# Kernel optimization log

Measured on AMD Instinct MI355X. Metric: run time of the kernel, lower is better.

## Reference

```python
import jax, jax.numpy as jnp
import numpy as np

N = 100000   # nodes
F_IN = 128   # node features
H = 32       # hidden size (hard-coded in module)


def setup_inputs() -> dict:
    key = jax.random.key(0)
    ks = jax.random.split(key, 20)
    inp = {
        'x': jax.random.normal(ks[0], (N, F_IN), dtype=jnp.float32),
        'edge_index': jax.random.randint(ks[1], (2, 3200000), 0, N, dtype=jnp.int64),
        'edge_weight': jax.random.uniform(ks[2], (3200000,), dtype=jnp.float32),
        'prev_hidden_state': jax.random.normal(ks[3], (N, H), dtype=jnp.float32),
    }
    s = 1.0 / np.sqrt(F_IN)
    s2 = 1.0 / np.sqrt(2 * H)
    sh = 1.0 / np.sqrt(H)
    # GCNConv weights (in->H) + bias, for gates z, r, h
    for i, g in enumerate(['z', 'r', 'h']):
        inp[f'Wc_{g}'] = jax.random.uniform(ks[4 + i], (F_IN, H), minval=-s, maxval=s, dtype=jnp.float32)
        inp[f'bc_{g}'] = jnp.zeros((H,), dtype=jnp.float32)
        # torch Linear(2H -> H): weight [H, 2H], bias [H]
        inp[f'Wl_{g}'] = jax.random.uniform(ks[8 + i], (H, 2 * H), minval=-s2, maxval=s2, dtype=jnp.float32)
        inp[f'bl_{g}'] = jax.random.uniform(ks[12 + i], (H,), minval=-s2, maxval=s2, dtype=jnp.float32)
    inp['W_head'] = jax.random.uniform(ks[16], (1, H), minval=-sh, maxval=sh, dtype=jnp.float32)
    inp['b_head'] = jax.random.uniform(ks[17], (1,), minval=-sh, maxval=sh, dtype=jnp.float32)
    return inp


def _gcn_norm(edge_index, edge_weight):
    # add self-loops with weight 1, symmetric GCN normalization
    loop = jnp.arange(N, dtype=edge_index.dtype)
    row = jnp.concatenate([edge_index[0], loop])
    col = jnp.concatenate([edge_index[1], loop])
    w = jnp.concatenate([edge_weight, jnp.ones((N,), dtype=edge_weight.dtype)])
    deg = jax.ops.segment_sum(w, col, num_segments=N)
    dinv = jnp.where(deg > 0, jax.lax.rsqrt(jnp.where(deg > 0, deg, 1.0)), 0.0)
    norm = dinv[row] * w * dinv[col]
    return row, col, norm


def _gcn_conv(x, W, b, row, col, norm):
    xw = x @ W                                   # [N, H]
    agg = jax.ops.segment_sum(norm[:, None] * xw[row], col, num_segments=N)
    return agg + b


def reference(x, edge_index, edge_weight, prev_hidden_state,
              Wc_z, bc_z, Wl_z, bl_z,
              Wc_r, bc_r, Wl_r, bl_r,
              Wc_h, bc_h, Wl_h, bl_h,
              W_head, b_head):
    row, col, norm = _gcn_norm(edge_index, edge_weight)
    Hprev = prev_hidden_state

    cz = _gcn_conv(x, Wc_z, bc_z, row, col, norm)
    Z = jax.nn.sigmoid(jnp.concatenate([cz, Hprev], axis=1) @ Wl_z.T + bl_z)

    cr = _gcn_conv(x, Wc_r, bc_r, row, col, norm)
    R = jax.nn.sigmoid(jnp.concatenate([cr, Hprev], axis=1) @ Wl_r.T + bl_r)

    ch = _gcn_conv(x, Wc_h, bc_h, row, col, norm)
    Ht = jnp.tanh(jnp.concatenate([ch, Hprev * R], axis=1) @ Wl_h.T + bl_h)

    Hnew = Z * Hprev + (1.0 - Z) * Ht
    y = jax.nn.relu(Hnew) @ W_head.T + b_head    # [N, 1]
    return (y, Hnew)
```

## Files before the change

### kernel.cpp

```cpp
#include <hip/hip_runtime.h>

#define NN 100000
#define FIN 128
#define HD 32
#define EE 3200000
#define NBUK 391
#define EPB 6144
#define NBLK ((EE + EPB - 1) / EPB)

typedef unsigned int uint;
typedef unsigned short ushort;
typedef float vfloat4 __attribute__((ext_vector_type(4)));

__device__ __forceinline__ ushort f2bf(float f) {
    uint b = __float_as_uint(f);
    return (ushort)((b + 0x7FFFu + ((b >> 16) & 1u)) >> 16);
}
__device__ __forceinline__ float bf2f(ushort u) {
    return __uint_as_float(((uint)u) << 16);
}

__device__ __forceinline__ int load_idx32(const int* __restrict__ ei, long long pos, int is64) {
    return is64 ? __builtin_nontemporal_load(ei + pos * 2)
                : __builtin_nontemporal_load(ei + pos);
}

__global__ __launch_bounds__(256) void passA_hist(const int* __restrict__ ei,
                                                  int* __restrict__ blockhist,
                                                  int* __restrict__ flag) {
    __shared__ int hist[NBUK];
    __shared__ int sis64;
    int tid = threadIdx.x, blk = blockIdx.x;
    for (int b = tid; b < NBUK; b += 256) hist[b] = 0;
    if (tid < 64) {
        uint v = 0;
#pragma unroll
        for (int r = 0; r < 4; r++) v |= ((const uint*)ei)[2 * (tid + 64 * r) + 1];
        unsigned long long nz = __ballot(v != 0u);
        if (tid == 0) sis64 = (nz == 0ULL) ? 1 : 0;
    }
    __syncthreads();
    int is64 = sis64;
    if (blk == 0 && tid == 0) *flag = is64;
    int e0 = blk * EPB, e1 = e0 + EPB; if (e1 > EE) e1 = EE;
    for (int e = e0 + tid; e < e1; e += 256) {
        int col = load_idx32(ei, (long long)EE + e, is64);
        atomicAdd(&hist[col >> 8], 1);
    }
    __syncthreads();
    for (int b = tid; b < NBUK; b += 256) blockhist[blk * NBUK + b] = hist[b];
}

__global__ void scan_bucket(const int* __restrict__ blockhist, int* __restrict__ off_local,
                            int* __restrict__ total) {
    int b = blockIdx.x;
    int l = threadIdx.x;
    int run = 0;
    for (int c = 0; c < NBLK; c += 64) {
        int blk = c + l;
        int v = (blk < NBLK) ? blockhist[blk * NBUK + b] : 0;
        int incl = v;
#pragma unroll
        for (int d = 1; d < 64; d <<= 1) {
            int t = __shfl_up(incl, d, 64);
            if (l >= d) incl += t;
        }
        if (blk < NBLK) off_local[blk * NBUK + b] = run + (incl - v);
        run += __shfl(incl, 63, 64);
    }
    if (l == 0) total[b] = run;
}

__global__ void scan_total(const int* __restrict__ total, int* __restrict__ bstart) {
    __shared__ int sd[512];
    int t = threadIdx.x;
    int v = (t < NBUK) ? total[t] : 0;
    sd[t] = v;
    __syncthreads();
    for (int off = 1; off < 512; off <<= 1) {
        int x = (t >= off) ? sd[t - off] : 0;
        __syncthreads();
        sd[t] += x;
        __syncthreads();
    }
    if (t < NBUK) bstart[t] = sd[t] - v;
    if (t == NBUK - 1) bstart[NBUK] = sd[t];
}

__global__ __launch_bounds__(512) void sortC_kernel(const int* __restrict__ ei,
                                                    const float* __restrict__ wt,
                                                    const int* __restrict__ bstart,
                                                    const int* __restrict__ off_local,
                                                    const int* __restrict__ blockhist,
                                                    uint2* __restrict__ erec2,
                                                    const int* __restrict__ flag) {
    __shared__ uint2 lrec[EPB];
    __shared__ int lcombo[NBUK];
    __shared__ int lcur[NBUK];
    int tid = threadIdx.x, blk = blockIdx.x;
    if (tid < 64) {
        int run = 0;
        for (int c = 0; c < NBUK; c += 64) {
            int b = c + tid;
            int v = (b < NBUK) ? blockhist[blk * NBUK + b] : 0;
            int incl = v;
#pragma unroll
            for (int d = 1; d < 64; d <<= 1) {
                int t2 = __shfl_up(incl, d, 64);
                if (tid >= d) incl += t2;
            }
            if (b < NBUK) {
                int ls = run + incl - v;
                lcur[b] = ls;
                lcombo[b] = bstart[b] + off_local[blk * NBUK + b] - ls;
            }
            run += __shfl(incl, 63, 64);
        }
    }
    __syncthreads();
    int is64 = *flag;
    int e0 = blk * EPB, e1 = e0 + EPB; if (e1 > EE) e1 = EE;
    for (int e = e0 + tid; e < e1; e += 512) {
        int row = load_idx32(ei, e, is64);
        int col = load_idx32(ei, (long long)EE + e, is64);
        uint nb = __float_as_uint(__builtin_nontemporal_load(wt + e));
        uint enc = ((nb + 0x8000u) >> 16) & 0x7FFFu;
        int pos = atomicAdd(&lcur[col >> 8], 1);
        uint2 r; r.x = (uint)row | (enc << 17); r.y = (uint)col;
        lrec[pos] = r;
    }
    __syncthreads();
    int m = e1 - e0;
    for (int slot = tid; slot < m; slot += 512) {
        uint2 r = lrec[slot];
        int gpos = lcombo[r.y >> 8] + slot;
        erec2[gpos] = r;
    }
}

__global__ __launch_bounds__(512) void passB_fine(const uint2* __restrict__ erec2,
                                                  const int* __restrict__ bstart,
                                                  uint* __restrict__ erecF,
                                                  int* __restrict__ estart, int* __restrict__ cnt,
                                                  float* __restrict__ dinv) {
    __shared__ int hist[256];
    __shared__ float wsum[256];
    __shared__ int off[256];
    __shared__ int cur[256];
    __shared__ int sd[256];
    int t = threadIdx.x, b = blockIdx.x;
    if (t < 256) { hist[t] = 0; wsum[t] = 0.f; }
    __syncthreads();
    int e0 = bstart[b], e1 = bstart[b + 1];
    for (int e = e0 + t; e < e1; e += 512) {
        uint2 r = erec2[e];
        int cl = (int)(r.y & 255u);
        atomicAdd(&hist[cl], 1);
        atomicAdd(&wsum[cl], __uint_as_float((r.x >> 17) << 16));
    }
    __syncthreads();
    int v = 0;
    if (t < 256) { v = hist[t]; sd[t] = v; }
    __syncthreads();
    for (int o = 1; o < 256; o <<= 1) {
        int x = (t >= o && t < 256) ? sd[t - o] : 0;
        __syncthreads();
        if (t < 256) sd[t] += x;
        __syncthreads();
    }
    if (t < 256) {
        off[t] = sd[t] - v;
        cur[t] = 0;
        int node = b * 256 + t;
        if (node < NN) {
            estart[node] = e0 + off[t];
            cnt[node] = v;
            dinv[node] = rsqrtf(1.0f + wsum[t]);
        }
    }
    __syncthreads();
    for (int e = e0 + t; e < e1; e += 512) {
        uint2 r = erec2[e];
        int cl = (int)(r.y & 255u);
        int p = atomicAdd(&cur[cl], 1);
        erecF[e0 + off[cl] + p] = r.x;
    }
}

__global__ __launch_bounds__(256) void gemm_xw_kernel(
        const float* __restrict__ x,
        const float* __restrict__ Wz, const float* __restrict__ Wr, const float* __restrict__ Wh,
        const float* __restrict__ dinv,
        ushort* __restrict__ xw16) {
    __shared__ float Bs[128 * 96];
    __shared__ float AsT[8 * 128];
    int tid = threadIdx.x;
    int tx = tid & 31, ty = tid >> 5;
    int rowBase = blockIdx.x * 128;

    for (int e = tid; e < 4096; e += 256) { int k = e >> 5, c = e & 31; Bs[k * 96 + c]      = Wz[e]; }
    for (int e = tid; e < 4096; e += 256) { int k = e >> 5, c = e & 31; Bs[k * 96 + 32 + c] = Wr[e]; }
    for (int e = tid; e < 4096; e += 256) { int k = e >> 5, c = e & 31; Bs[k * 96 + 64 + c] = Wh[e]; }

    float acc0[16], acc1[16], acc2[16];
#pragma unroll
    for (int r = 0; r < 16; r++) { acc0[r] = 0.f; acc1[r] = 0.f; acc2[r] = 0.f; }

    int lr = tid >> 1;
    int lc = (tid & 1) * 4;
    for (int k0 = 0; k0 < 128; k0 += 8) {
        __syncthreads();
        int gr = rowBase + lr;
        vfloat4 a4 = (vfloat4)(0.f);
        if (gr < NN) a4 = __builtin_nontemporal_load((const vfloat4*)(x + (long long)gr * FIN + k0 + lc));
        AsT[(lc + 0) * 128 + lr] = a4.x;
        AsT[(lc + 1) * 128 + lr] = a4.y;
        AsT[(lc + 2) * 128 + lr] = a4.z;
        AsT[(lc + 3) * 128 + lr] = a4.w;
        __syncthreads();
#pragma unroll
        for (int kk = 0; kk < 8; kk++) {
            float b0 = Bs[(k0 + kk) * 96 + tx];
            float b1 = Bs[(k0 + kk) * 96 + 32 + tx];
            float b2 = Bs[(k0 + kk) * 96 + 64 + tx];
            const float4* ap = (const float4*)(AsT + kk * 128 + ty * 16);
            float4 a0 = ap[0], a1 = ap[1], a2 = ap[2], a3 = ap[3];
            float av[16] = {a0.x,a0.y,a0.z,a0.w, a1.x,a1.y,a1.z,a1.w,
                            a2.x,a2.y,a2.z,a2.w, a3.x,a3.y,a3.z,a3.w};
#pragma unroll
            for (int r = 0; r < 16; r++) {
                acc0[r] = fmaf(av[r], b0, acc0[r]);
                acc1[r] = fmaf(av[r], b1, acc1[r]);
                acc2[r] = fmaf(av[r], b2, acc2[r]);
            }
        }
    }
#pragma unroll
    for (int r = 0; r < 16; r++) {
        int gr = rowBase + ty * 16 + r;
        if (gr < NN) {
            float di = dinv[gr];
            ushort* o = xw16 + (long long)gr * 96;
            uint zr = (uint)f2bf(acc0[r] * di) | ((uint)f2bf(acc1[r] * di) << 16);
            *(uint*)(o + 2 * tx) = zr;
            o[64 + tx] = f2bf(acc2[r] * di);
        }
    }
}

__global__ __launch_bounds__(512) void agg_gate_kernel(
        const uint* __restrict__ erecF, const int* __restrict__ estart, const int* __restrict__ cnt,
        const ushort* __restrict__ xw16, const float* __restrict__ dinv,
        const float* __restrict__ hprev,
        const float* __restrict__ bcz, const float* __restrict__ bcr, const float* __restrict__ bch,
        const float* __restrict__ Wlz, const float* __restrict__ blz,
        const float* __restrict__ Wlr, const float* __restrict__ blr,
        const float* __restrict__ Wlh, const float* __restrict__ blh,
        const float* __restrict__ Whead, const float* __restrict__ bhead,
        float* __restrict__ y, float* __restrict__ hnew) {
    __shared__ float WzT[64 * 32], WrT[64 * 32], WhT[64 * 32];
    __shared__ float czs[16][32], crs[16][32], chs[16][32], hps[16][32], rhs[16][32];
    __shared__ uint rwsh[16][32];
    int tid = threadIdx.x;
    for (int e2 = tid; e2 < 2048; e2 += 512) {
        int jj = e2 >> 6, k = e2 & 63;
        WzT[k * 32 + jj] = Wlz[e2];
        WrT[k * 32 + jj] = Wlr[e2];
        WhT[k * 32 + jj] = Wlh[e2];
    }
    int s = tid >> 5, j = tid & 31;
    int i = blockIdx.x * 16 + s;
    int beg = estart[i], c = cnt[i], end = beg + c;

    const char* xwb = (const char*)xw16;
    uint jo4 = 4u * (uint)j;
    uint jo2 = 128u + 2u * (uint)j;

    float cz = 0.f, cr = 0.f, ch = 0.f;
    int e = beg + j;
    uint vcur = (e < end) ? __builtin_nontemporal_load(erecF + e) : 0u;
    __syncthreads();

#define REC(vv, aa, hh)                                                    \
    {                                                                      \
        float w_ = __uint_as_float(((vv) >> 17) << 16);                    \
        cz = fmaf(w_, __uint_as_float((aa) << 16), cz);                    \
        cr = fmaf(w_, __uint_as_float((aa) & 0xFFFF0000u), cr);            \
        ch = fmaf(w_, bf2f(hh), ch);                                       \
    }

    for (int base = beg; base < end; base += 32) {
        rwsh[s][j] = vcur;
        int en = base + 32 + j;
        uint vnext = (en < end) ? __builtin_nontemporal_load(erecF + en) : 0u;
        int mm = end - base; if (mm > 32) mm = 32;
        int t = 0;
        for (; t + 8 <= mm; t += 8) {
            uint v0 = rwsh[s][t + 0], v1 = rwsh[s][t + 1], v2 = rwsh[s][t + 2], v3 = rwsh[s][t + 3];
            uint v4 = rwsh[s][t + 4], v5 = rwsh[s][t + 5], v6 = rwsh[s][t + 6], v7 = rwsh[s][t + 7];
            uint b0 = (v0 & 0x1FFFFu) * 192u, b1 = (v1 & 0x1FFFFu) * 192u;
            uint b2 = (v2 & 0x1FFFFu) * 192u, b3 = (v3 & 0x1FFFFu) * 192u;
            uint b4 = (v4 & 0x1FFFFu) * 192u, b5 = (v5 & 0x1FFFFu) * 192u;
            uint b6 = (v6 & 0x1FFFFu) * 192u, b7 = (v7 & 0x1FFFFu) * 192u;
            uint a0 = *(const uint*)(xwb + b0 + jo4);
            uint a1 = *(const uint*)(xwb + b1 + jo4);
            uint a2 = *(const uint*)(xwb + b2 + jo4);
            uint a3 = *(const uint*)(xwb + b3 + jo4);
            uint a4 = *(const uint*)(xwb + b4 + jo4);
            uint a5 = *(const uint*)(xwb + b5 + jo4);
            uint a6 = *(const uint*)(xwb + b6 + jo4);
            uint a7 = *(const uint*)(xwb + b7 + jo4);
            ushort h0 = *(const ushort*)(xwb + b0 + jo2);
            ushort h1 = *(const ushort*)(xwb + b1 + jo2);
            ushort h2 = *(const ushort*)(xwb + b2 + jo2);
            ushort h3 = *(const ushort*)(xwb + b3 + jo2);
            ushort h4 = *(const ushort*)(xwb + b4 + jo2);
            ushort h5 = *(const ushort*)(xwb + b5 + jo2);
            ushort h6 = *(const ushort*)(xwb + b6 + jo2);
            ushort h7 = *(const ushort*)(xwb + b7 + jo2);
            REC(v0, a0, h0) REC(v1, a1, h1) REC(v2, a2, h2) REC(v3, a3, h3)
            REC(v4, a4, h4) REC(v5, a5, h5) REC(v6, a6, h6) REC(v7, a7, h7)
        }
        for (; t + 4 <= mm; t += 4) {
            uint v0 = rwsh[s][t + 0], v1 = rwsh[s][t + 1], v2 = rwsh[s][t + 2], v3 = rwsh[s][t + 3];
            uint b0 = (v0 & 0x1FFFFu) * 192u, b1 = (v1 & 0x1FFFFu) * 192u;
            uint b2 = (v2 & 0x1FFFFu) * 192u, b3 = (v3 & 0x1FFFFu) * 192u;
            uint a0 = *(const uint*)(xwb + b0 + jo4);
            uint a1 = *(const uint*)(xwb + b1 + jo4);
            uint a2 = *(const uint*)(xwb + b2 + jo4);
            uint a3 = *(const uint*)(xwb + b3 + jo4);
            ushort h0 = *(const ushort*)(xwb + b0 + jo2);
            ushort h1 = *(const ushort*)(xwb + b1 + jo2);
            ushort h2 = *(const ushort*)(xwb + b2 + jo2);
            ushort h3 = *(const ushort*)(xwb + b3 + jo2);
            REC(v0, a0, h0) REC(v1, a1, h1) REC(v2, a2, h2) REC(v3, a3, h3)
        }
        for (; t < mm; t++) {
            uint v0 = rwsh[s][t];
            uint b0 = (v0 & 0x1FFFFu) * 192u;
            uint a0 = *(const uint*)(xwb + b0 + jo4);
            ushort h0 = *(const ushort*)(xwb + b0 + jo2);
            REC(v0, a0, h0)
        }
        vcur = vnext;
    }
#undef REC

    float di = dinv[i];
    uint bi = (uint)i * 192u;
    uint zri = *(const uint*)(xwb + bi + jo4);
    float hself = bf2f(*(const ushort*)(xwb + bi + jo2));
    czs[s][j] = fmaf(di, cz + __uint_as_float(zri << 16), bcz[j]);
    crs[s][j] = fmaf(di, cr + __uint_as_float(zri & 0xFFFF0000u), bcr[j]);
    chs[s][j] = fmaf(di, ch + hself, bch[j]);
    float hp = __builtin_nontemporal_load(hprev + (long long)i * HD + j);
    hps[s][j] = hp;

    float az = blz[j], arv = blr[j];
#pragma unroll
    for (int k = 0; k < 32; k++) {
        az  = fmaf(WzT[k * 32 + j], czs[s][k], az);
        arv = fmaf(WrT[k * 32 + j], crs[s][k], arv);
    }
#pragma unroll
    for (int k = 0; k < 32; k++) {
        float v = hps[s][k];
        az  = fmaf(WzT[(k + 32) * 32 + j], v, az);
        arv = fmaf(WrT[(k + 32) * 32 + j], v, arv);
    }
    float Z = 1.f / (1.f + __expf(-az));
    float R = 1.f / (1.f + __expf(-arv));
    rhs[s][j] = hp * R;

    float ah = blh[j];
#pragma unroll
    for (int k = 0; k < 32; k++) ah = fmaf(WhT[k * 32 + j], chs[s][k], ah);
#pragma unroll
    for (int k = 0; k < 32; k++) ah = fmaf(WhT[(k + 32) * 32 + j], rhs[s][k], ah);
    float Ht = tanhf(ah);
    float hn = Z * hp + (1.f - Z) * Ht;
    float yv = fmaxf(hn, 0.f) * Whead[j];
#pragma unroll
    for (int m = 16; m; m >>= 1) yv += __shfl_xor(yv, m, 32);
    __builtin_nontemporal_store(hn, hnew + (long long)i * HD + j);
    if (j == 0) y[i] = yv + bhead[0];
}

extern "C" void kernel_launch(void* const* d_in, const int* in_sizes, int n_in,
                              void* d_out, int out_size, void* d_ws, size_t ws_size,
                              hipStream_t stream) {
    const float* x     = (const float*)d_in[0];
    const int*   ei    = (const int*)d_in[1];
    const float* wt    = (const float*)d_in[2];
    const float* hprev = (const float*)d_in[3];
    const float* Wcz = (const float*)d_in[4],  *bcz = (const float*)d_in[5];
    const float* Wlz = (const float*)d_in[6],  *blz = (const float*)d_in[7];
    const float* Wcr = (const float*)d_in[8],  *bcr = (const float*)d_in[9];
    const float* Wlr = (const float*)d_in[10], *blr = (const float*)d_in[11];
    const float* Wch = (const float*)d_in[12], *bch = (const float*)d_in[13];
    const float* Wlh = (const float*)d_in[14], *blh = (const float*)d_in[15];
    const float* Whead = (const float*)d_in[16], *bhead = (const float*)d_in[17];

    float* out_y = (float*)d_out;
    float* out_h = (float*)d_out + NN;

    float* ws = (float*)d_ws;
    float* dinv      = ws;
    int*   estart    = (int*)(ws + NN);
    int*   cnt       = (int*)(ws + 2LL * NN);
    int*   bstart    = (int*)(ws + 3LL * NN);
    int*   total     = (int*)(ws + 3LL * NN + 512);
    int*   blockhist = (int*)(ws + 3LL * NN + 1024);
    int*   off_local = (int*)(ws + 3LL * NN + 205024);
    int*   flag      = (int*)(ws + 3LL * NN + 409024);
    ushort* xw16     = (ushort*)(ws + 3LL * NN + 409056);
    uint2*  erec2    = (uint2*)(ws + 51LL * NN + 409056);
    uint*   erecF    = (uint*)(ws + 51LL * NN + 409056 + 2LL * EE);

    passA_hist<<<NBLK, 256, 0, stream>>>(ei, blockhist, flag);
    scan_bucket<<<NBUK, 64, 0, stream>>>(blockhist, off_local, total);
    scan_total<<<1, 512, 0, stream>>>(total, bstart);
    sortC_kernel<<<NBLK, 512, 0, stream>>>(ei, wt, bstart, off_local, blockhist, erec2, flag);
    passB_fine<<<NBUK, 512, 0, stream>>>(erec2, bstart, erecF, estart, cnt, dinv);
    gemm_xw_kernel<<<(NN + 127) / 128, 256, 0, stream>>>(x, Wcz, Wcr, Wch, dinv, xw16);
    agg_gate_kernel<<<NN / 16, 512, 0, stream>>>(
        erecF, estart, cnt, xw16, dinv, hprev, bcz, bcr, bch,
        Wlz, blz, Wlr, blr, Wlh, blh, Whead, bhead, out_y, out_h);
}
```

Measured before the change: 514.0 us.

## Pad xw rows to 256 bytes and gather z/r/h with one 8-byte load

```diff
diff --git a/kernel.cpp b/kernel.cpp
--- a/kernel.cpp
+++ b/kernel.cpp
@@ -240,10 +240,11 @@
         int gr = rowBase + ty * 16 + r;
         if (gr < NN) {
             float di = dinv[gr];
-            ushort* o = xw16 + (long long)gr * 96;
-            uint zr = (uint)f2bf(acc0[r] * di) | ((uint)f2bf(acc1[r] * di) << 16);
-            *(uint*)(o + 2 * tx) = zr;
-            o[64 + tx] = f2bf(acc2[r] * di);
+            ushort* o = xw16 + (long long)gr * 128;
+            uint w0 = (uint)f2bf(acc0[r] * di) | ((uint)f2bf(acc1[r] * di) << 16);
+            uint w1 = (uint)f2bf(acc2[r] * di);
+            uint2 pk; pk.x = w0; pk.y = w1;
+            *(uint2*)(o + 4 * tx) = pk;
         }
     }
 }
@@ -273,20 +274,19 @@
     int beg = estart[i], c = cnt[i], end = beg + c;
 
     const char* xwb = (const char*)xw16;
-    uint jo4 = 4u * (uint)j;
-    uint jo2 = 128u + 2u * (uint)j;
+    uint jo8 = 8u * (uint)j;
 
     float cz = 0.f, cr = 0.f, ch = 0.f;
     int e = beg + j;
     uint vcur = (e < end) ? __builtin_nontemporal_load(erecF + e) : 0u;
     __syncthreads();
 
-#define REC(vv, aa, hh)                                                    \
+#define REC(vv, dd)                                                        \
     {                                                                      \
         float w_ = __uint_as_float(((vv) >> 17) << 16);                    \
-        cz = fmaf(w_, __uint_as_float((aa) << 16), cz);                    \
-        cr = fmaf(w_, __uint_as_float((aa) & 0xFFFF0000u), cr);            \
-        ch = fmaf(w_, bf2f(hh), ch);                                       \
+        cz = fmaf(w_, __uint_as_float((dd).x << 16), cz);                  \
+        cr = fmaf(w_, __uint_as_float((dd).x & 0xFFFF0000u), cr);          \
+        ch = fmaf(w_, __uint_as_float((dd).y << 16), ch);                  \
     }
 
     for (int base = beg; base < end; base += 32) {
@@ -295,64 +295,31 @@
         uint vnext = (en < end) ? __builtin_nontemporal_load(erecF + en) : 0u;
         int mm = end - base; if (mm > 32) mm = 32;
         int t = 0;
-        for (; t + 8 <= mm; t += 8) {
-            uint v0 = rwsh[s][t + 0], v1 = rwsh[s][t + 1], v2 = rwsh[s][t + 2], v3 = rwsh[s][t + 3];
-            uint v4 = rwsh[s][t + 4], v5 = rwsh[s][t + 5], v6 = rwsh[s][t + 6], v7 = rwsh[s][t + 7];
-            uint b0 = (v0 & 0x1FFFFu) * 192u, b1 = (v1 & 0x1FFFFu) * 192u;
-            uint b2 = (v2 & 0x1FFFFu) * 192u, b3 = (v3 & 0x1FFFFu) * 192u;
-            uint b4 = (v4 & 0x1FFFFu) * 192u, b5 = (v5 & 0x1FFFFu) * 192u;
-            uint b6 = (v6 & 0x1FFFFu) * 192u, b7 = (v7 & 0x1FFFFu) * 192u;
-            uint a0 = *(const uint*)(xwb + b0 + jo4);
-            uint a1 = *(const uint*)(xwb + b1 + jo4);
-            uint a2 = *(const uint*)(xwb + b2 + jo4);
-            uint a3 = *(const uint*)(xwb + b3 + jo4);
-            uint a4 = *(const uint*)(xwb + b4 + jo4);
-            uint a5 = *(const uint*)(xwb + b5 + jo4);
-            uint a6 = *(const uint*)(xwb + b6 + jo4);
-            uint a7 = *(const uint*)(xwb + b7 + jo4);
-            ushort h0 = *(const ushort*)(xwb + b0 + jo2);
-            ushort h1 = *(const ushort*)(xwb + b1 + jo2);
-            ushort h2 = *(const ushort*)(xwb + b2 + jo2);
-            ushort h3 = *(const ushort*)(xwb + b3 + jo2);
-            ushort h4 = *(const ushort*)(xwb + b4 + jo2);
-            ushort h5 = *(const ushort*)(xwb + b5 + jo2);
-            ushort h6 = *(const ushort*)(xwb + b6 + jo2);
-            ushort h7 = *(const ushort*)(xwb + b7 + jo2);
-            REC(v0, a0, h0) REC(v1, a1, h1) REC(v2, a2, h2) REC(v3, a3, h3)
-            REC(v4, a4, h4) REC(v5, a5, h5) REC(v6, a6, h6) REC(v7, a7, h7)
-        }
         for (; t + 4 <= mm; t += 4) {
             uint v0 = rwsh[s][t + 0], v1 = rwsh[s][t + 1], v2 = rwsh[s][t + 2], v3 = rwsh[s][t + 3];
-            uint b0 = (v0 & 0x1FFFFu) * 192u, b1 = (v1 & 0x1FFFFu) * 192u;
-            uint b2 = (v2 & 0x1FFFFu) * 192u, b3 = (v3 & 0x1FFFFu) * 192u;
-            uint a0 = *(const uint*)(xwb + b0 + jo4);
-            uint a1 = *(const uint*)(xwb + b1 + jo4);
-            uint a2 = *(const uint*)(xwb + b2 + jo4);
-            uint a3 = *(const uint*)(xwb + b3 + jo4);
-            ushort h0 = *(const ushort*)(xwb + b0 + jo2);
-            ushort h1 = *(const ushort*)(xwb + b1 + jo2);
-            ushort h2 = *(const ushort*)(xwb + b2 + jo2);
-            ushort h3 = *(const ushort*)(xwb + b3 + jo2);
-            REC(v0, a0, h0) REC(v1, a1, h1) REC(v2, a2, h2) REC(v3, a3, h3)
+            uint b0 = (v0 & 0x1FFFFu) * 256u, b1 = (v1 & 0x1FFFFu) * 256u;
+            uint b2 = (v2 & 0x1FFFFu) * 256u, b3 = (v3 & 0x1FFFFu) * 256u;
+            uint2 d0 = *(const uint2*)(xwb + b0 + jo8);
+            uint2 d1 = *(const uint2*)(xwb + b1 + jo8);
+            uint2 d2 = *(const uint2*)(xwb + b2 + jo8);
+            uint2 d3 = *(const uint2*)(xwb + b3 + jo8);
+            REC(v0, d0) REC(v1, d1) REC(v2, d2) REC(v3, d3)
         }
         for (; t < mm; t++) {
             uint v0 = rwsh[s][t];
-            uint b0 = (v0 & 0x1FFFFu) * 192u;
-            uint a0 = *(const uint*)(xwb + b0 + jo4);
-            ushort h0 = *(const ushort*)(xwb + b0 + jo2);
-            REC(v0, a0, h0)
+            uint b0 = (v0 & 0x1FFFFu) * 256u;
+            uint2 d0 = *(const uint2*)(xwb + b0 + jo8);
+            REC(v0, d0)
         }
         vcur = vnext;
     }
 #undef REC
 
     float di = dinv[i];
-    uint bi = (uint)i * 192u;
-    uint zri = *(const uint*)(xwb + bi + jo4);
-    float hself = bf2f(*(const ushort*)(xwb + bi + jo2));
-    czs[s][j] = fmaf(di, cz + __uint_as_float(zri << 16), bcz[j]);
-    crs[s][j] = fmaf(di, cr + __uint_as_float(zri & 0xFFFF0000u), bcr[j]);
-    chs[s][j] = fmaf(di, ch + hself, bch[j]);
+    uint2 dself = *(const uint2*)(xwb + (uint)i * 256u + jo8);
+    czs[s][j] = fmaf(di, cz + __uint_as_float(dself.x << 16), bcz[j]);
+    crs[s][j] = fmaf(di, cr + __uint_as_float(dself.x & 0xFFFF0000u), bcr[j]);
+    chs[s][j] = fmaf(di, ch + __uint_as_float(dself.y << 16), bch[j]);
     float hp = __builtin_nontemporal_load(hprev + (long long)i * HD + j);
     hps[s][j] = hp;
 
@@ -413,9 +380,9 @@
     int*   blockhist = (int*)(ws + 3LL * NN + 1024);
     int*   off_local = (int*)(ws + 3LL * NN + 205024);
     int*   flag      = (int*)(ws + 3LL * NN + 409024);
-    ushort* xw16     = (ushort*)(ws + 3LL * NN + 409056);
-    uint2*  erec2    = (uint2*)(ws + 51LL * NN + 409056);
-    uint*   erecF    = (uint*)(ws + 51LL * NN + 409056 + 2LL * EE);
+    uint2*  erec2    = (uint2*)(ws + 3LL * NN + 409056);
+    ushort* xw16     = (ushort*)erec2;
+    uint*   erecF    = (uint*)(ws + 3LL * NN + 409056 + 2LL * EE);
 
     passA_hist<<<NBLK, 256, 0, stream>>>(ei, blockhist, flag);
     scan_bucket<<<NBUK, 64, 0, stream>>>(blockhist, off_local, total);
```

New measurement: 542.0 us. 5.4% more time.
